# Kernel tuning notes

Measured on AMD Instinct MI355X. Metric: run time of the kernel, lower is better.

## Reference

```python
import jax, jax.numpy as jnp
import numpy as np


def setup_inputs() -> dict:
    key = jax.random.key(0)
    k1, k2 = jax.random.split(key)
    B, T = 16, 2048
    n_fft = 1024
    hop_length = 256
    win_length = 1024
    N = n_fft // 2 + 1  # 513 rfft bins
    spec_real = jax.random.normal(k1, (B, N, T), dtype=jnp.float32)
    spec_imag = jax.random.normal(k2, (B, N, T), dtype=jnp.float32)
    # periodic Hann window (torch.hann_window default)
    n = jnp.arange(win_length, dtype=jnp.float32)
    window = 0.5 * (1.0 - jnp.cos(2.0 * jnp.pi * n / win_length))
    return {
        "spec_real": spec_real,
        "spec_imag": spec_imag,
        "window": window,
        "n_fft": n_fft,
        "hop_length": hop_length,
        "win_length": win_length,
    }


def reference(spec_real, spec_imag, window, n_fft, hop_length, win_length):
    pad = (win_length - hop_length) // 2
    B, N, T = spec_real.shape
    spec = spec_real + 1j * spec_imag  # [B, N, T] complex
    # irfft along freq dim with 'backward' norm (jnp default): [B, n_fft, T]
    ifft = jnp.fft.irfft(spec, n=n_fft, axis=1)
    ifft = ifft * window[None, :, None]  # windowed frames
    L = (T - 1) * hop_length + win_length  # overlap-add output length
    # scatter indices: sample positions of each frame, shape [win_length, T]
    idx = jnp.arange(T)[None, :] * hop_length + jnp.arange(win_length)[:, None]
    y = jnp.zeros((B, L), dtype=ifft.dtype).at[:, idx].add(ifft)
    y = y[:, pad:L - pad]
    # window-squared envelope, same overlap-add pattern
    wsq = jnp.broadcast_to((window * window)[:, None], (win_length, T))
    env = jnp.zeros((L,), dtype=window.dtype).at[idx].add(wsq)[pad:L - pad]
    return y / env
```

## Files before the change

kernel.cpp:

```cpp
#include <hip/hip_runtime.h>

#define BB 16
#define TT 2048
#define NROW 513
#define HOP 256
#define OUTLB 524288
#define FTO 28
#define SPAN (FTO*HOP)
#define TILES 74
#define RZ 513

__device__ __forceinline__ int brev9(int k){ return (int)(__brev((unsigned)k)>>23); }
__device__ __forceinline__ int zidx(int f,int m){ return f*RZ + (m ^ ((m>>4)&28) ^ (f<<2)); }

__global__ __launch_bounds__(512,4) void istft_fused(
    const float* __restrict__ sr, const float* __restrict__ si,
    const float* __restrict__ win, float* __restrict__ out)
{
  __shared__ float2 zc[8*RZ];
  __shared__ float2 ttab[256];
  __shared__ float2 wtab[512];

  const int tid  = threadIdx.x;
  const int b    = blockIdx.x / TILES;
  const int tile = blockIdx.x % TILES;
  const int Tbase= tile*FTO - 2;

  if (tid < 256){
    float s,c; __sincosf((float)tid*0.012271846303085130f,&s,&c);
    ttab[tid]=make_float2(c,s);
  }
  wtab[tid] = ((const float2*)win)[tid];

  float2 acc[7];
  #pragma unroll
  for (int i=0;i<7;++i) acc[i]=make_float2(0.f,0.f);

  const int f  = tid & 7;
  const int pp = tid >> 3;
  const float* srb = sr + (size_t)b*NROW*TT;
  const float* sib = si + (size_t)b*NROW*TT;

  float ctw[4], stw[4];
  #pragma unroll
  for (int cc=0;cc<4;++cc){
    __sincosf((float)(cc*64+pp)*0.006135923151542565f,&stw[cc],&ctw[cc]);
  }

  auto storeZ = [&](int cc, float ar,float ai,float br,float bi,float cr,float ci){
    int k = cc*64+pp;
    if (k==0){
      zc[zidx(f,0)] = make_float2(0.5f*(ar+br), 0.5f*(ar-br));
      zc[zidx(f,1)] = make_float2(cr, -ci);
    } else {
      float Er=0.5f*(ar+br), Ei=0.5f*(ai-bi);
      float Dr=0.5f*(ar-br), Di=0.5f*(ai+bi);
      float Or=Dr*ctw[cc]-Di*stw[cc], Oi=Dr*stw[cc]+Di*ctw[cc];
      zc[zidx(f,brev9(k))]     = make_float2(Er-Oi, Ei+Or);
      zc[zidx(f,brev9(512-k))] = make_float2(Er+Oi, Or-Ei);
    }
  };

  auto do_fft = [&](){
    #pragma unroll
    for (int st=0; st<4; ++st){
      __syncthreads();
      const int h = 1<<(2*st);
      #pragma unroll
      for (int i=0;i<2;++i){
        int q   = pp + 64*i;
        int ilo = q & (h-1);
        int base= ((q>>(2*st))<<(2*st+2)) + ilo;
        float2 w1 = ttab[ilo<<(8-2*st)];
        float2 w2 = ttab[ilo<<(7-2*st)];
        float2 e0=zc[zidx(f,base)],     e1=zc[zidx(f,base+h)];
        float2 e2=zc[zidx(f,base+2*h)], e3=zc[zidx(f,base+3*h)];
        float t1r=e1.x*w1.x-e1.y*w1.y, t1i=e1.x*w1.y+e1.y*w1.x;
        float t3r=e3.x*w1.x-e3.y*w1.y, t3i=e3.x*w1.y+e3.y*w1.x;
        float arr=e0.x+t1r, ari=e0.y+t1i, brr=e0.x-t1r, bri=e0.y-t1i;
        float crr=e2.x+t3r, cri=e2.y+t3i, drr=e2.x-t3r, dri=e2.y-t3i;
        float cwr=crr*w2.x-cri*w2.y, cwi=crr*w2.y+cri*w2.x;
        float dwr=drr*w2.x-dri*w2.y, dwi=drr*w2.y+dri*w2.x;
        zc[zidx(f,base)]     = make_float2(arr+cwr, ari+cwi);
        zc[zidx(f,base+2*h)] = make_float2(arr-cwr, ari-cwi);
        zc[zidx(f,base+h)]   = make_float2(brr-dwi, bri+dwr);
        zc[zidx(f,base+3*h)] = make_float2(brr+dwi, bri-dwr);
      }
    }
    __syncthreads();
    #pragma unroll
    for (int i=0;i<4;++i){
      int q = pp + 64*i;
      float2 tw = ttab[q];
      float2 u = zc[zidx(f,q)], v = zc[zidx(f,q+256)];
      float tr=v.x*tw.x-v.y*tw.y, ti=v.x*tw.y+v.y*tw.x;
      zc[zidx(f,q)]     = make_float2(u.x+tr, u.y+ti);
      zc[zidx(f,q+256)] = make_float2(u.x-tr, u.y-ti);
    }
  };

  auto do_gather = [&](int c){
    __syncthreads();
    const int jb = 896 - 2048*c;
    #pragma unroll
    for (int i=0;i<7;++i){
      int j0 = 2*(tid + 512*i) + jb;
      int s_lo = max(0, (j0-768)>>8);
      int s_hi = min(7, j0>>8);
      for (int s=s_lo; s<=s_hi; ++s){
        int m0 = (j0 - 256*s)>>1;
        float2 v = zc[zidx(s,m0)];
        float2 w = wtab[m0];
        acc[i].x += v.x*w.x;
        acc[i].y += v.y*w.y;
      }
    }
  };

  for (int half=0; half<2; ++half){
    const int c0  = 2*half;
    const int ta  = Tbase + 8*c0 + f;
    const int tb_ = ta + 8;
    const int tca = min(max(ta ,0),TT-1);
    const int tcb = min(max(tb_,0),TT-1);
    const float ma  = (ta >=0 && ta <TT)?(1.f/512.f):0.f;
    const float mb2 = (tb_>=0 && tb_<TT)?(1.f/512.f):0.f;

    float sAr[4],sAi[4],sBr[4],sBi[4];
    float sCr=0.f, sCi=0.f;

    __syncthreads();
    #pragma unroll
    for (int cc=0;cc<4;++cc){
      int k = cc*64+pp;
      const float* pr  = srb + (size_t)k*TT;
      const float* pi_ = sib + (size_t)k*TT;
      const float* qr  = srb + (size_t)(512-k)*TT;
      const float* qi  = sib + (size_t)(512-k)*TT;
      float ar0=pr [tca], ar1=pr [tcb];
      float ai0=pi_[tca], ai1=pi_[tcb];
      float br0=qr [tca], br1=qr [tcb];
      float bi0=qi [tca], bi1=qi [tcb];
      sAr[cc]=ar1; sAi[cc]=ai1; sBr[cc]=br1; sBi[cc]=bi1;
      float cr0=0.f, ci0=0.f;
      if (cc==0 && pp==0){
        const float* rr = srb + (size_t)256*TT;
        const float* ri = sib + (size_t)256*TT;
        cr0 = rr[tca]; sCr = rr[tcb];
        ci0 = ri[tca]; sCi = ri[tcb];
      }
      storeZ(cc, ar0*ma, ai0*ma, br0*ma, bi0*ma, cr0*ma, ci0*ma);
    }
    do_fft();
    do_gather(c0);

    __syncthreads();
    #pragma unroll
    for (int cc=0;cc<4;++cc){
      storeZ(cc, sAr[cc]*mb2, sAi[cc]*mb2, sBr[cc]*mb2, sBi[cc]*mb2, sCr*mb2, sCi*mb2);
    }
    do_fft();
    do_gather(c0+1);
  }

  const bool edge = (tile==0)|(tile==TILES-1);
  float* outb = out + (size_t)b*OUTLB;
  const int gbase = tile*SPAN;
  #pragma unroll
  for (int i=0;i<7;++i){
    int p0 = 2*(tid + 512*i);
    int gs = gbase + p0;
    if (gs < OUTLB){
      float2 r = acc[i];
      if (!edge){
        r.x *= (2.f/3.f); r.y *= (2.f/3.f);
      } else {
        #pragma unroll
        for (int e=0;e<2;++e){
          int l = gbase + 384 + p0 + e;
          int j0 = l & 255, tb = l >> 8;
          float env=0.f;
          #pragma unroll
          for (int mm=0;mm<4;++mm){
            int t2 = tb-mm;
            if (t2>=0 && t2<TT){
              float wv = 0.5f-0.5f*__cosf((float)(j0+256*mm)*0.006135923151542565f);
              env += wv*wv;
            }
          }
          ((float*)&r)[e] /= env;
        }
      }
      *(float2*)(outb+gs) = r;
    }
  }
}

extern "C" void kernel_launch(void* const* d_in, const int* in_sizes, int n_in,
                              void* d_out, int out_size, void* d_ws, size_t ws_size,
                              hipStream_t stream) {
  const float* sr = (const float*)d_in[0];
  const float* si = (const float*)d_in[1];
  const float* w  = (const float*)d_in[2];
  float* out = (float*)d_out;
  istft_fused<<<BB*TILES, 512, 0, stream>>>(sr, si, w, out);
}
```

Baseline: 249.3 us.

## Replace radix-4/2 shared-memory FFT with three radix-8 passes

The 512-point complex FFT changes from four radix-4 stages plus a radix-2 stage (five barriers) to three radix-8 stages with digit-reversed input ordering and a new XOR swizzle. Twiddles are now computed on the fly with __sincosf, replacing the shared twiddle table and precomputed per-thread values. The goal is fewer LDS round trips and barriers per FFT. In exchange it adds more transcendental instructions and more live registers per thread, which could hurt occupancy under the 512x4 launch bounds.

```diff
diff --git a/kernel.cpp b/kernel.cpp
--- a/kernel.cpp
+++ b/kernel.cpp
@@ -8,17 +8,40 @@
 #define FTO 28
 #define SPAN (FTO*HOP)
 #define TILES 74
-#define RZ 513
-
-__device__ __forceinline__ int brev9(int k){ return (int)(__brev((unsigned)k)>>23); }
-__device__ __forceinline__ int zidx(int f,int m){ return f*RZ + (m ^ ((m>>4)&28) ^ (f<<2)); }
+#define RZ2 514
+
+__device__ __forceinline__ int dig8rev(int k){ return ((k&7)<<6) | (k&56) | (k>>6); }
+__device__ __forceinline__ int zidx(int f,int m){ return f*RZ2 + (m ^ ((m>>3)&7) ^ ((m>>6)&7)); }
+
+#define CADD(a,b) make_float2((a).x+(b).x,(a).y+(b).y)
+#define CSUB(a,b) make_float2((a).x-(b).x,(a).y-(b).y)
+
+__device__ __forceinline__ void dft8(float2 (&y)[8]){
+  const float C7 = 0.70710678118654752f;
+  float2 s0=CADD(y[0],y[4]), s1=CSUB(y[0],y[4]);
+  float2 s2=CADD(y[2],y[6]), s3=CSUB(y[2],y[6]);
+  float2 u0=CADD(y[1],y[5]), u1=CSUB(y[1],y[5]);
+  float2 u2=CADD(y[3],y[7]), u3=CSUB(y[3],y[7]);
+  float2 E0=CADD(s0,s2), E2=CSUB(s0,s2);
+  float2 E1=make_float2(s1.x - s3.y, s1.y + s3.x);
+  float2 E3=make_float2(s1.x + s3.y, s1.y - s3.x);
+  float2 O0=CADD(u0,u2), O2=CSUB(u0,u2);
+  float2 O1=make_float2(u1.x - u3.y, u1.y + u3.x);
+  float2 O3=make_float2(u1.x + u3.y, u1.y - u3.x);
+  float2 T1=make_float2(C7*(O1.x-O1.y), C7*(O1.x+O1.y));
+  float2 T2=make_float2(-O2.y, O2.x);
+  float2 T3=make_float2(C7*(-O3.x-O3.y), C7*(O3.x-O3.y));
+  y[0]=CADD(E0,O0); y[4]=CSUB(E0,O0);
+  y[1]=CADD(E1,T1); y[5]=CSUB(E1,T1);
+  y[2]=CADD(E2,T2); y[6]=CSUB(E2,T2);
+  y[3]=CADD(E3,T3); y[7]=CSUB(E3,T3);
+}
 
 __global__ __launch_bounds__(512,4) void istft_fused(
     const float* __restrict__ sr, const float* __restrict__ si,
     const float* __restrict__ win, float* __restrict__ out)
 {
-  __shared__ float2 zc[8*RZ];
-  __shared__ float2 ttab[256];
+  __shared__ float2 zc[8*RZ2];
   __shared__ float2 wtab[512];
 
   const int tid  = threadIdx.x;
@@ -26,10 +49,6 @@
   const int tile = blockIdx.x % TILES;
   const int Tbase= tile*FTO - 2;
 
-  if (tid < 256){
-    float s,c; __sincosf((float)tid*0.012271846303085130f,&s,&c);
-    ttab[tid]=make_float2(c,s);
-  }
   wtab[tid] = ((const float2*)win)[tid];
 
   float2 acc[7];
@@ -41,61 +60,62 @@
   const float* srb = sr + (size_t)b*NROW*TT;
   const float* sib = si + (size_t)b*NROW*TT;
 
-  float ctw[4], stw[4];
-  #pragma unroll
-  for (int cc=0;cc<4;++cc){
-    __sincosf((float)(cc*64+pp)*0.006135923151542565f,&stw[cc],&ctw[cc]);
-  }
-
   auto storeZ = [&](int cc, float ar,float ai,float br,float bi,float cr,float ci){
     int k = cc*64+pp;
     if (k==0){
       zc[zidx(f,0)] = make_float2(0.5f*(ar+br), 0.5f*(ar-br));
-      zc[zidx(f,1)] = make_float2(cr, -ci);
+      zc[zidx(f,4)] = make_float2(cr, -ci);
     } else {
+      float s_,c_; __sincosf((float)k*0.006135923151542565f,&s_,&c_);
       float Er=0.5f*(ar+br), Ei=0.5f*(ai-bi);
       float Dr=0.5f*(ar-br), Di=0.5f*(ai+bi);
-      float Or=Dr*ctw[cc]-Di*stw[cc], Oi=Dr*stw[cc]+Di*ctw[cc];
-      zc[zidx(f,brev9(k))]     = make_float2(Er-Oi, Ei+Or);
-      zc[zidx(f,brev9(512-k))] = make_float2(Er+Oi, Or-Ei);
+      float Or=Dr*c_-Di*s_, Oi=Dr*s_+Di*c_;
+      zc[zidx(f,dig8rev(k))]     = make_float2(Er-Oi, Ei+Or);
+      zc[zidx(f,dig8rev(512-k))] = make_float2(Er+Oi, Or-Ei);
     }
   };
 
   auto do_fft = [&](){
-    #pragma unroll
-    for (int st=0; st<4; ++st){
-      __syncthreads();
-      const int h = 1<<(2*st);
-      #pragma unroll
-      for (int i=0;i<2;++i){
-        int q   = pp + 64*i;
-        int ilo = q & (h-1);
-        int base= ((q>>(2*st))<<(2*st+2)) + ilo;
-        float2 w1 = ttab[ilo<<(8-2*st)];
-        float2 w2 = ttab[ilo<<(7-2*st)];
-        float2 e0=zc[zidx(f,base)],     e1=zc[zidx(f,base+h)];
-        float2 e2=zc[zidx(f,base+2*h)], e3=zc[zidx(f,base+3*h)];
-        float t1r=e1.x*w1.x-e1.y*w1.y, t1i=e1.x*w1.y+e1.y*w1.x;
-        float t3r=e3.x*w1.x-e3.y*w1.y, t3i=e3.x*w1.y+e3.y*w1.x;
-        float arr=e0.x+t1r, ari=e0.y+t1i, brr=e0.x-t1r, bri=e0.y-t1i;
-        float crr=e2.x+t3r, cri=e2.y+t3i, drr=e2.x-t3r, dri=e2.y-t3i;
-        float cwr=crr*w2.x-cri*w2.y, cwi=crr*w2.y+cri*w2.x;
-        float dwr=drr*w2.x-dri*w2.y, dwi=drr*w2.y+dri*w2.x;
-        zc[zidx(f,base)]     = make_float2(arr+cwr, ari+cwi);
-        zc[zidx(f,base+2*h)] = make_float2(arr-cwr, ari-cwi);
-        zc[zidx(f,base+h)]   = make_float2(brr-dwi, bri+dwr);
-        zc[zidx(f,base+3*h)] = make_float2(brr+dwi, bri-dwr);
-      }
-    }
-    __syncthreads();
-    #pragma unroll
-    for (int i=0;i<4;++i){
-      int q = pp + 64*i;
-      float2 tw = ttab[q];
-      float2 u = zc[zidx(f,q)], v = zc[zidx(f,q+256)];
-      float tr=v.x*tw.x-v.y*tw.y, ti=v.x*tw.y+v.y*tw.x;
-      zc[zidx(f,q)]     = make_float2(u.x+tr, u.y+ti);
-      zc[zidx(f,q+256)] = make_float2(u.x-tr, u.y-ti);
+    float2 y[8];
+    __syncthreads();
+    {
+      const int base = pp<<3;
+      #pragma unroll
+      for (int t=0;t<8;++t) y[t]=zc[zidx(f,base+t)];
+      dft8(y);
+      #pragma unroll
+      for (int t=0;t<8;++t) zc[zidx(f,base+t)]=y[t];
+    }
+    __syncthreads();
+    {
+      const int ilo = pp&7, base = ((pp>>3)<<6) + ilo;
+      #pragma unroll
+      for (int t=0;t<8;++t) y[t]=zc[zidx(f,base+8*t)];
+      const float a1 = (float)ilo * 0.09817477042468103f;
+      #pragma unroll
+      for (int t=1;t<8;++t){
+        float s_,c_; __sincosf(a1*(float)t,&s_,&c_);
+        float xr=y[t].x, xi=y[t].y;
+        y[t]=make_float2(xr*c_-xi*s_, xr*s_+xi*c_);
+      }
+      dft8(y);
+      #pragma unroll
+      for (int t=0;t<8;++t) zc[zidx(f,base+8*t)]=y[t];
+    }
+    __syncthreads();
+    {
+      #pragma unroll
+      for (int t=0;t<8;++t) y[t]=zc[zidx(f,pp+64*t)];
+      const float a2 = (float)pp * 0.012271846303085130f;
+      #pragma unroll
+      for (int t=1;t<8;++t){
+        float s_,c_; __sincosf(a2*(float)t,&s_,&c_);
+        float xr=y[t].x, xi=y[t].y;
+        y[t]=make_float2(xr*c_-xi*s_, xr*s_+xi*c_);
+      }
+      dft8(y);
+      #pragma unroll
+      for (int t=0;t<8;++t) zc[zidx(f,pp+64*t)]=y[t];
     }
   };
 
```

Result: slower. 370.0 us (+48.5%).

## Batch 16 frames per FFT pass with float2 loads and XCD-aware block mapping

Applied to the files above, without the earlier changes.

Each pass now holds 16 frames in shared memory instead of 8, so a tile needs two FFT passes and two syncthreads groups rather than four. Spectrum reads become float2 loads of two adjacent frames. The shared twiddle and window tables are replaced by on-the-fly sincos and per-thread window registers. A new swizzle changes LDS bank mapping, and block indices are remapped so that consecutive tiles land on the same XCD. Shared memory per block rises to 64KB, which may limit occupancy, and the extra sincos calls add ALU work.

```diff
diff --git a/kernel.cpp b/kernel.cpp
--- a/kernel.cpp
+++ b/kernel.cpp
@@ -8,29 +8,27 @@
 #define FTO 28
 #define SPAN (FTO*HOP)
 #define TILES 74
-#define RZ 513
+#define NWG (BB*TILES)
+#define CPX (NWG/8)
 
 __device__ __forceinline__ int brev9(int k){ return (int)(__brev((unsigned)k)>>23); }
-__device__ __forceinline__ int zidx(int f,int m){ return f*RZ + (m ^ ((m>>4)&28) ^ (f<<2)); }
+__device__ __forceinline__ int zidx(int r,int m){
+  int s = m ^ ((m>>3)&7) ^ ((m>>6)&7);
+  return (r<<9) + (s ^ ((2*r)&15));
+}
 
 __global__ __launch_bounds__(512,4) void istft_fused(
     const float* __restrict__ sr, const float* __restrict__ si,
     const float* __restrict__ win, float* __restrict__ out)
 {
-  __shared__ float2 zc[8*RZ];
-  __shared__ float2 ttab[256];
-  __shared__ float2 wtab[512];
+  __shared__ float2 zc[16*512];
 
-  const int tid  = threadIdx.x;
-  const int b    = blockIdx.x / TILES;
-  const int tile = blockIdx.x % TILES;
+  const int tid = threadIdx.x;
+  const int d    = blockIdx.x;
+  const int L    = (d & 7)*CPX + (d >> 3);
+  const int b    = L / TILES;
+  const int tile = L % TILES;
   const int Tbase= tile*FTO - 2;
-
-  if (tid < 256){
-    float s,c; __sincosf((float)tid*0.012271846303085130f,&s,&c);
-    ttab[tid]=make_float2(c,s);
-  }
-  wtab[tid] = ((const float2*)win)[tid];
 
   float2 acc[7];
   #pragma unroll
@@ -41,126 +39,117 @@
   const float* srb = sr + (size_t)b*NROW*TT;
   const float* sib = si + (size_t)b*NROW*TT;
 
-  float ctw[4], stw[4];
+  const int r_w = (tid + 64) & 127;
+  float2 wreg[4];
   #pragma unroll
-  for (int cc=0;cc<4;++cc){
-    __sincosf((float)(cc*64+pp)*0.006135923151542565f,&stw[cc],&ctw[cc]);
-  }
+  for (int j=0;j<4;++j) wreg[j] = ((const float2*)win)[r_w + 128*j];
 
-  auto storeZ = [&](int cc, float ar,float ai,float br,float bi,float cr,float ci){
-    int k = cc*64+pp;
+  auto storeZ = [&](int row, int k, float ar,float ai,float br,float bi,
+                    float cr,float ci, float s_, float c_){
     if (k==0){
-      zc[zidx(f,0)] = make_float2(0.5f*(ar+br), 0.5f*(ar-br));
-      zc[zidx(f,1)] = make_float2(cr, -ci);
+      zc[zidx(row,0)] = make_float2(0.5f*(ar+br), 0.5f*(ar-br));
+      zc[zidx(row,1)] = make_float2(cr, -ci);
     } else {
       float Er=0.5f*(ar+br), Ei=0.5f*(ai-bi);
       float Dr=0.5f*(ar-br), Di=0.5f*(ai+bi);
-      float Or=Dr*ctw[cc]-Di*stw[cc], Oi=Dr*stw[cc]+Di*ctw[cc];
-      zc[zidx(f,brev9(k))]     = make_float2(Er-Oi, Ei+Or);
-      zc[zidx(f,brev9(512-k))] = make_float2(Er+Oi, Or-Ei);
+      float Or=Dr*c_-Di*s_, Oi=Dr*s_+Di*c_;
+      zc[zidx(row,brev9(k))]     = make_float2(Er-Oi, Ei+Or);
+      zc[zidx(row,brev9(512-k))] = make_float2(Er+Oi, Or-Ei);
     }
   };
 
-  auto do_fft = [&](){
+  for (int half=0; half<2; ++half){
+    const int T0 = Tbase + 16*half;
+    const int ta = T0 + 2*f;
+    const int tp = min(max(ta,0),TT-2);
+    const float m0_ = (ta>=0   && ta  <TT)?(1.f/512.f):0.f;
+    const float m1_ = (ta+1>=0 && ta+1<TT)?(1.f/512.f):0.f;
+
+    __syncthreads();
+    #pragma unroll
+    for (int cc=0;cc<4;++cc){
+      const int k = cc*64+pp;
+      const float2 vRk = *(const float2*)(srb + (size_t)k*TT + tp);
+      const float2 vIk = *(const float2*)(sib + (size_t)k*TT + tp);
+      const float2 vRq = *(const float2*)(srb + (size_t)(512-k)*TT + tp);
+      const float2 vIq = *(const float2*)(sib + (size_t)(512-k)*TT + tp);
+      float2 vRc=make_float2(0.f,0.f), vIc=make_float2(0.f,0.f);
+      if (cc==0 && pp==0){
+        vRc = *(const float2*)(srb + (size_t)256*TT + tp);
+        vIc = *(const float2*)(sib + (size_t)256*TT + tp);
+      }
+      float s_,c_; __sincosf((float)k*0.006135923151542565f,&s_,&c_);
+      storeZ(2*f,   k, vRk.x*m0_, vIk.x*m0_, vRq.x*m0_, vIq.x*m0_, vRc.x*m0_, vIc.x*m0_, s_, c_);
+      storeZ(2*f+1, k, vRk.y*m1_, vIk.y*m1_, vRq.y*m1_, vIq.y*m1_, vRc.y*m1_, vIc.y*m1_, s_, c_);
+    }
+
     #pragma unroll
     for (int st=0; st<4; ++st){
       __syncthreads();
       const int h = 1<<(2*st);
       #pragma unroll
       for (int i=0;i<2;++i){
-        int q   = pp + 64*i;
-        int ilo = q & (h-1);
-        int base= ((q>>(2*st))<<(2*st+2)) + ilo;
-        float2 w1 = ttab[ilo<<(8-2*st)];
-        float2 w2 = ttab[ilo<<(7-2*st)];
-        float2 e0=zc[zidx(f,base)],     e1=zc[zidx(f,base+h)];
-        float2 e2=zc[zidx(f,base+2*h)], e3=zc[zidx(f,base+3*h)];
-        float t1r=e1.x*w1.x-e1.y*w1.y, t1i=e1.x*w1.y+e1.y*w1.x;
-        float t3r=e3.x*w1.x-e3.y*w1.y, t3i=e3.x*w1.y+e3.y*w1.x;
-        float arr=e0.x+t1r, ari=e0.y+t1i, brr=e0.x-t1r, bri=e0.y-t1i;
-        float crr=e2.x+t3r, cri=e2.y+t3i, drr=e2.x-t3r, dri=e2.y-t3i;
-        float cwr=crr*w2.x-cri*w2.y, cwi=crr*w2.y+cri*w2.x;
-        float dwr=drr*w2.x-dri*w2.y, dwi=drr*w2.y+dri*w2.x;
-        zc[zidx(f,base)]     = make_float2(arr+cwr, ari+cwi);
-        zc[zidx(f,base+2*h)] = make_float2(arr-cwr, ari-cwi);
-        zc[zidx(f,base+h)]   = make_float2(brr-dwi, bri+dwr);
-        zc[zidx(f,base+3*h)] = make_float2(brr+dwi, bri-dwr);
+        const int q   = pp + 64*i;
+        const int ilo = q & (h-1);
+        const int base= ((q>>(2*st))<<(2*st+2)) + ilo;
+        float2 w1, w2;
+        if (st==0){ w1=make_float2(1.f,0.f); w2=w1; }
+        else {
+          float s1,c1,s2,c2;
+          __sincosf((float)(ilo<<(8-2*st))*0.012271846303085130f,&s1,&c1);
+          __sincosf((float)(ilo<<(7-2*st))*0.012271846303085130f,&s2,&c2);
+          w1=make_float2(c1,s1); w2=make_float2(c2,s2);
+        }
+        #pragma unroll
+        for (int ch=0; ch<2; ++ch){
+          const int r = ch*8 + f;
+          float2 e0=zc[zidx(r,base)],     e1=zc[zidx(r,base+h)];
+          float2 e2=zc[zidx(r,base+2*h)], e3=zc[zidx(r,base+3*h)];
+          float t1r=e1.x*w1.x-e1.y*w1.y, t1i=e1.x*w1.y+e1.y*w1.x;
+          float t3r=e3.x*w1.x-e3.y*w1.y, t3i=e3.x*w1.y+e3.y*w1.x;
+          float arr=e0.x+t1r, ari=e0.y+t1i, brr=e0.x-t1r, bri=e0.y-t1i;
+          float crr=e2.x+t3r, cri=e2.y+t3i, drr=e2.x-t3r, dri=e2.y-t3i;
+          float cwr=crr*w2.x-cri*w2.y, cwi=crr*w2.y+cri*w2.x;
+          float dwr=drr*w2.x-dri*w2.y, dwi=drr*w2.y+dri*w2.x;
+          zc[zidx(r,base)]     = make_float2(arr+cwr, ari+cwi);
+          zc[zidx(r,base+2*h)] = make_float2(arr-cwr, ari-cwi);
+          zc[zidx(r,base+h)]   = make_float2(brr-dwi, bri+dwr);
+          zc[zidx(r,base+3*h)] = make_float2(brr+dwi, bri-dwr);
+        }
       }
     }
     __syncthreads();
     #pragma unroll
     for (int i=0;i<4;++i){
-      int q = pp + 64*i;
-      float2 tw = ttab[q];
-      float2 u = zc[zidx(f,q)], v = zc[zidx(f,q+256)];
-      float tr=v.x*tw.x-v.y*tw.y, ti=v.x*tw.y+v.y*tw.x;
-      zc[zidx(f,q)]     = make_float2(u.x+tr, u.y+ti);
-      zc[zidx(f,q+256)] = make_float2(u.x-tr, u.y-ti);
+      const int q = pp + 64*i;
+      float sq,cq; __sincosf((float)q*0.012271846303085130f,&sq,&cq);
+      #pragma unroll
+      for (int ch=0; ch<2; ++ch){
+        const int r = ch*8 + f;
+        float2 u = zc[zidx(r,q)], v = zc[zidx(r,q+256)];
+        float tr=v.x*cq-v.y*sq, ti=v.x*sq+v.y*cq;
+        zc[zidx(r,q)]     = make_float2(u.x+tr, u.y+ti);
+        zc[zidx(r,q+256)] = make_float2(u.x-tr, u.y-ti);
+      }
     }
-  };
 
-  auto do_gather = [&](int c){
     __syncthreads();
-    const int jb = 896 - 2048*c;
+    const int boff = 448 - 2048*half;
     #pragma unroll
     for (int i=0;i<7;++i){
-      int j0 = 2*(tid + 512*i) + jb;
-      int s_lo = max(0, (j0-768)>>8);
-      int s_hi = min(7, j0>>8);
-      for (int s=s_lo; s<=s_hi; ++s){
-        int m0 = (j0 - 256*s)>>1;
-        float2 v = zc[zidx(s,m0)];
-        float2 w = wtab[m0];
-        acc[i].x += v.x*w.x;
-        acc[i].y += v.y*w.y;
+      const int base = tid + 512*i + boff;
+      const int Sb   = (base - r_w) >> 7;
+      #pragma unroll
+      for (int j=0;j<4;++j){
+        const int S = Sb - j;
+        if (S >= 0 && S < 16){
+          const int m0 = r_w + 128*j;
+          float2 v = zc[zidx(S,m0)];
+          acc[i].x += v.x*wreg[j].x;
+          acc[i].y += v.y*wreg[j].y;
+        }
       }
     }
-  };
-
-  for (int half=0; half<2; ++half){
-    const int c0  = 2*half;
-    const int ta  = Tbase + 8*c0 + f;
-    const int tb_ = ta + 8;
-    const int tca = min(max(ta ,0),TT-1);
-    const int tcb = min(max(tb_,0),TT-1);
-    const float ma  = (ta >=0 && ta <TT)?(1.f/512.f):0.f;
-    const float mb2 = (tb_>=0 && tb_<TT)?(1.f/512.f):0.f;
-
-    float sAr[4],sAi[4],sBr[4],sBi[4];
-    float sCr=0.f, sCi=0.f;
-
-    __syncthreads();
-    #pragma unroll
-    for (int cc=0;cc<4;++cc){
-      int k = cc*64+pp;
-      const float* pr  = srb + (size_t)k*TT;
-      const float* pi_ = sib + (size_t)k*TT;
-      const float* qr  = srb + (size_t)(512-k)*TT;
-      const float* qi  = sib + (size_t)(512-k)*TT;
-      float ar0=pr [tca], ar1=pr [tcb];
-      float ai0=pi_[tca], ai1=pi_[tcb];
-      float br0=qr [tca], br1=qr [tcb];
-      float bi0=qi [tca], bi1=qi [tcb];
-      sAr[cc]=ar1; sAi[cc]=ai1; sBr[cc]=br1; sBi[cc]=bi1;
-      float cr0=0.f, ci0=0.f;
-      if (cc==0 && pp==0){
-        const float* rr = srb + (size_t)256*TT;
-        const float* ri = sib + (size_t)256*TT;
-        cr0 = rr[tca]; sCr = rr[tcb];
-        ci0 = ri[tca]; sCi = ri[tcb];
-      }
-      storeZ(cc, ar0*ma, ai0*ma, br0*ma, bi0*ma, cr0*ma, ci0*ma);
-    }
-    do_fft();
-    do_gather(c0);
-
-    __syncthreads();
-    #pragma unroll
-    for (int cc=0;cc<4;++cc){
-      storeZ(cc, sAr[cc]*mb2, sAi[cc]*mb2, sBr[cc]*mb2, sBi[cc]*mb2, sCr*mb2, sCi*mb2);
-    }
-    do_fft();
-    do_gather(c0+1);
   }
 
   const bool edge = (tile==0)|(tile==TILES-1);
@@ -203,5 +192,5 @@
   const float* si = (const float*)d_in[1];
   const float* w  = (const float*)d_in[2];
   float* out = (float*)d_out;
-  istft_fused<<<BB*TILES, 512, 0, stream>>>(sr, si, w, out);
+  istft_fused<<<NWG, 512, 0, stream>>>(sr, si, w, out);
 }
```

Result: slower. 278.8 us (+11.9%).
